# Optimization experiments

Measured on AMD Instinct MI355X. Metric: run time of the kernel, lower is better.

## Reference

```python
import jax, jax.numpy as jnp
import numpy as np

B, CIN, COUT, MODES, T = 64, 32, 32, 16, 1024
DT = 0.01  # uniform time-grid spacing (grid_x_train in the original repo)
SCALE = 1.0 / (CIN * COUT)


def setup_inputs() -> dict:
    key = jax.random.key(0)
    k = jax.random.split(key, 5)
    x = jax.random.normal(k[0], (B, CIN, T), dtype=jnp.float32)
    t = jnp.arange(T, dtype=jnp.float32) * np.float32(DT)
    # torch.rand with dtype=cfloat samples real and imag parts ~ U[0,1)
    pole_real = SCALE * jax.random.uniform(k[1], (CIN, COUT, MODES), dtype=jnp.float32)
    pole_imag = SCALE * jax.random.uniform(k[2], (CIN, COUT, MODES), dtype=jnp.float32)
    res_real = SCALE * jax.random.uniform(k[3], (CIN, COUT, MODES), dtype=jnp.float32)
    res_imag = SCALE * jax.random.uniform(k[4], (CIN, COUT, MODES), dtype=jnp.float32)
    return {"x": x, "t": t, "pole_real": pole_real, "pole_imag": pole_imag,
            "res_real": res_real, "res_imag": res_imag}


def reference(x, t, pole_real, pole_imag, res_real, res_imag):
    n = x.shape[-1]  # == T == t.shape[0]
    pole = (pole_real + 1j * pole_imag).astype(jnp.complex64)      # [i,o,m]
    residue = (res_real + 1j * res_imag).astype(jnp.complex64)     # [i,o,m]

    alpha = jnp.fft.fft(x)  # [b,i,T] complex64
    dt = t[1] - t[0]
    two_pi = np.float32(2.0 * np.pi)
    # lambda0 = fftfreq(T, dt) * 2*pi*1j  (fftfreq(T)/dt keeps dt traced-friendly)
    lam = ((jnp.fft.fftfreq(n).astype(jnp.float32) / dt) * two_pi * 1j).astype(jnp.complex64)  # [T]

    # Hw[x,i,o,k] = residue[i,o,k] / (lambda[x] - pole[i,o,k])
    Hw = residue[None, :, :, :] / (lam[:, None, None, None] - pole[None, :, :, :])  # [T,i,o,m]

    out1 = jnp.einsum('bix,xiok->box', alpha, Hw)    # [b,o,T]
    out2 = -jnp.einsum('bix,xiok->bok', alpha, Hw)   # [b,o,m]

    x1 = jnp.real(jnp.fft.ifft(out1, n=n))  # [b,o,T]

    # term2[i,o,m,z] = exp(pole[i,o,m] * t[z])
    term2 = jnp.exp(pole[:, :, :, None] * t.astype(jnp.complex64)[None, None, None, :])  # [i,o,m,T]
    # note: original einsum contracts out2's channel dim against term2's in-channel dim
    x2 = jnp.real(jnp.einsum('bix,ioxz->boz', out2, term2)) / n  # [b,o,T]

    return x1 + x2
```

## Files before the change

kernel.cpp:

```cpp
#include <hip/hip_runtime.h>

#define T_N   1024
#define B_N   64
#define CIN   32
#define COUT  32
#define MODES 16
#define DT    0.01f
#define PI_F  3.14159265358979323846f
#define W_SCALE 0.613592315154256f
#define W_NYQ  (-314.1592653589793f)

typedef short bf16x8 __attribute__((ext_vector_type(8)));
typedef float f32x4 __attribute__((ext_vector_type(4)));

__device__ __forceinline__ float fastrcp(float x) {
    float r;
    asm("v_rcp_f32 %0, %1" : "=v"(r) : "v"(x));
    return r;
}

__device__ __forceinline__ void bfsplit(float v, short* ph, short* pl) {
    unsigned int u = __float_as_uint(v);
    float lo = v - __uint_as_float(u & 0xFFFF0000u);
    *ph = (short)(u >> 16);
    *pl = (short)(__float_as_uint(lo) >> 16);
}

template <int SIGN>
__device__ __forceinline__ float2* fft1024_r4(float2* A, float2* B,
                                              const float2* TW, int tid) {
    float2* src = A;
    float2* dst = B;
    int m = 1;
#pragma unroll
    for (int s = 0; s < 5; ++s) {
        __syncthreads();
        int k  = tid & (m - 1);
        int jm = tid - k;
        float2 a = src[tid];
        float2 b = src[tid + 256];
        float2 c = src[tid + 512];
        float2 d = src[tid + 768];
        float2 t0 = make_float2(a.x + c.x, a.y + c.y);
        float2 t1 = make_float2(a.x - c.x, a.y - c.y);
        float2 t2 = make_float2(b.x + d.x, b.y + d.y);
        float2 t3 = make_float2(b.x - d.x, b.y - d.y);
        float2 it3 = (SIGN == 1) ? make_float2(-t3.y, t3.x)
                                 : make_float2(t3.y, -t3.x);
        float2 y0 = make_float2(t0.x + t2.x, t0.y + t2.y);
        float2 y2 = make_float2(t0.x - t2.x, t0.y - t2.y);
        float2 y1 = make_float2(t1.x + it3.x, t1.y + it3.y);
        float2 y3 = make_float2(t1.x - it3.x, t1.y - it3.y);
        float2 w1 = TW[jm];
        float2 w2 = TW[2 * jm];
        float2 w3 = TW[3 * jm];
        int ob = k + 4 * jm;
        dst[ob] = y0;
        dst[ob + m]     = make_float2(w1.x * y1.x - w1.y * y1.y,
                                      w1.x * y1.y + w1.y * y1.x);
        dst[ob + 2 * m] = make_float2(w2.x * y2.x - w2.y * y2.y,
                                      w2.x * y2.y + w2.y * y2.x);
        dst[ob + 3 * m] = make_float2(w3.x * y3.x - w3.y * y3.y,
                                      w3.x * y3.y + w3.y * y3.x);
        float2* t = src; src = dst; dst = t;
        m <<= 2;
    }
    __syncthreads();
    return src;
}

template <int SIGN>
__device__ __forceinline__ void build_tw4(float2* TW, int tid) {
#pragma unroll
    for (int r = 0; r < 4; ++r) {
        int a = tid + (r << 8);
        float sn, cs;
        __sincosf((float)SIGN * PI_F * (float)a * (1.0f / 512.0f), &sn, &cs);
        TW[a] = make_float2(cs, sn);
    }
}

__global__ __launch_bounds__(256) void k_fft_fwd(const float* __restrict__ x,
                                                 float2* __restrict__ alpha,
                                                 short* __restrict__ aHi,
                                                 short* __restrict__ aLo,
                                                 const float* __restrict__ pr,
                                                 const float* __restrict__ pim,
                                                 const float* __restrict__ rr,
                                                 const float* __restrict__ ri,
                                                 float4* __restrict__ pol4) {
    __shared__ float2 A[1024];
    __shared__ float2 Bb[1024];
    __shared__ float2 TW[1024];
    int row = blockIdx.x;
    int tid = threadIdx.x;
    build_tw4<-1>(TW, tid);
    const float* xr = x + (size_t)row * T_N;
#pragma unroll
    for (int r = 0; r < 4; ++r) {
        int j = tid + (r << 8);
        A[j] = make_float2(xr[j], 0.0f);
    }
    float2* R = fft1024_r4<-1>(A, Bb, TW, tid);
    float2* outp = alpha + (size_t)row * T_N;
#pragma unroll
    for (int r = 0; r < 4; ++r) {
        int j = tid + (r << 8);
        outp[j] = R[j];
    }
    size_t base = (size_t)row * 1024;
#pragma unroll
    for (int rr_ = 0; rr_ < 2; ++rr_) {
        int xj = tid + (rr_ << 8);
        float2 v = R[xj];
        float aR = v.x;
        float aI = (xj == 0) ? R[512].x : v.y;
        short h0, l0, h1, l1;
        bfsplit(aR, &h0, &l0);
        bfsplit(aI, &h1, &l1);
        aHi[base + xj * 2]     = h0;
        aHi[base + xj * 2 + 1] = h1;
        aLo[base + xj * 2]     = l0;
        aLo[base + xj * 2 + 1] = l1;
    }
    if (row < 64) {
        int idx = row * 256 + tid;
        pol4[idx] = make_float4(pr[idx], pim[idx], rr[idx], ri[idx]);
    }
}

__global__ __launch_bounds__(256) void k_transpose_hw(const float2* __restrict__ alpha,
                                                      unsigned int* __restrict__ aThU,
                                                      unsigned int* __restrict__ aTlU,
                                                      const float4* __restrict__ pol4,
                                                      float2* __restrict__ hw) {
    __shared__ float2 T[32 * 66];
    int bid = blockIdx.x;
    int tid = threadIdx.x;
    if (bid < 1024) {
        int i = bid >> 5, xt = bid & 31;
#pragma unroll
        for (int r = 0; r < 8; ++r) {
            int e = tid + (r << 8);
            int xx = e & 31, b = e >> 5;
            T[xx * 66 + b] = alpha[((size_t)(b * CIN + i)) * T_N + xt * 32 + xx];
        }
        __syncthreads();
#pragma unroll
        for (int r = 0; r < 8; ++r) {
            int e = tid + (r << 8);
            int b = e & 63, xx = e >> 6;
            float2 v = T[xx * 66 + b];
            short hR, lR, hI, lI;
            bfsplit(v.x, &hR, &lR);
            bfsplit(v.y, &hI, &lI);
            size_t idx = ((size_t)i * T_N + xt * 32 + xx) * B_N + b;
            aThU[idx] = (unsigned int)(unsigned short)hR |
                        ((unsigned int)(unsigned short)hI << 16);
            aTlU[idx] = (unsigned int)(unsigned short)lR |
                        ((unsigned int)(unsigned short)lI << 16);
        }
    } else {
        int xb = bid - 1024;
        int io0 = tid * 4;
        float wv[4];
#pragma unroll
        for (int xi = 0; xi < 4; ++xi) {
            int xg = xb * 4 + xi;
            int fx = xg - ((xg >= 512) ? 1024 : 0);
            wv[xi] = (float)fx * W_SCALE;
        }
        float accR[4][4], accI[4][4];
#pragma unroll
        for (int j = 0; j < 4; ++j) {
            const float4* pp = pol4 + (io0 + j) * 16;
            float4 p[16];
#pragma unroll
            for (int k = 0; k < 16; ++k) p[k] = pp[k];
#pragma unroll
            for (int xi = 0; xi < 4; ++xi) {
                float hr = 0.f, hi = 0.f;
#pragma unroll
                for (int k = 0; k < 16; ++k) {
                    float a = p[k].x, bI = p[k].y;
                    float d = wv[xi] - bI;
                    float inv = fastrcp(fmaf(d, d, a * a));
                    float vR = -a * inv, vI = -d * inv;
                    hr += p[k].z * vR - p[k].w * vI;
                    hi += p[k].z * vI + p[k].w * vR;
                }
                accR[xi][j] = hr;
                accI[xi][j] = hi;
            }
        }
#pragma unroll
        for (int xi = 0; xi < 4; ++xi) {
            float4* dst = (float4*)(hw + (size_t)(xb * 4 + xi) * 1024 + io0);
            dst[0] = make_float4(accR[xi][0], accI[xi][0], accR[xi][1], accI[xi][1]);
            dst[1] = make_float4(accR[xi][2], accI[xi][2], accR[xi][3], accI[xi][3]);
        }
    }
}

__global__ __launch_bounds__(256) void k_out1(const unsigned int* __restrict__ aThU,
                                              const unsigned int* __restrict__ aTlU,
                                              const float2* __restrict__ hw,
                                              float2* __restrict__ out1tmp) {
    __shared__ float sARe[32 * 64];
    __shared__ float sAIm[32 * 64];
    int x = blockIdx.x;
    int tid = threadIdx.x;

#pragma unroll
    for (int r = 0; r < 4; ++r) {
        int e = tid + (r << 8);
        int i = e >> 5, bp = e & 31;
        size_t base = ((size_t)i * T_N + x) * B_N + bp * 2;
        uint2 uh = *(const uint2*)&aThU[base];
        uint2 ul = *(const uint2*)&aTlU[base];
        float r0 = __uint_as_float(uh.x << 16) + __uint_as_float(ul.x << 16);
        float i0 = __uint_as_float(uh.x & 0xFFFF0000u) + __uint_as_float(ul.x & 0xFFFF0000u);
        float r1 = __uint_as_float(uh.y << 16) + __uint_as_float(ul.y << 16);
        float i1 = __uint_as_float(uh.y & 0xFFFF0000u) + __uint_as_float(ul.y & 0xFFFF0000u);
        *(float2*)&sARe[i * 64 + bp * 2] = make_float2(r0, r1);
        *(float2*)&sAIm[i * 64 + bp * 2] = make_float2(i0, i1);
    }
    __syncthreads();

    int o = tid & 31, bg = tid >> 5;
    const float2* hrow = hw + (size_t)x * 1024 + o;
    float accR[8] = {}, accI[8] = {};
#pragma unroll 4
    for (int i = 0; i < CIN; ++i) {
        float2 h = hrow[i * 32];
        float4 ar0 = *(const float4*)&sARe[i * 64 + bg * 8];
        float4 ar1 = *(const float4*)&sARe[i * 64 + bg * 8 + 4];
        float4 ai0 = *(const float4*)&sAIm[i * 64 + bg * 8];
        float4 ai1 = *(const float4*)&sAIm[i * 64 + bg * 8 + 4];
        float aR[8] = {ar0.x, ar0.y, ar0.z, ar0.w, ar1.x, ar1.y, ar1.z, ar1.w};
        float aI[8] = {ai0.x, ai0.y, ai0.z, ai0.w, ai1.x, ai1.y, ai1.z, ai1.w};
#pragma unroll
        for (int bb = 0; bb < 8; ++bb) {
            accR[bb] += aR[bb] * h.x - aI[bb] * h.y;
            accI[bb] += aR[bb] * h.y + aI[bb] * h.x;
        }
    }
#pragma unroll
    for (int bb = 0; bb < 8; ++bb) {
        out1tmp[(size_t)x * 2048 + (bg * 8 + bb) * 32 + o] =
            make_float2(accR[bb], accI[bb]);
    }
}

#define ABROW 40
__global__ __launch_bounds__(256) void k_out2m(const short* __restrict__ aHi,
                                               const short* __restrict__ aLo,
                                               const float* __restrict__ pr,
                                               const float* __restrict__ pim,
                                               const float* __restrict__ rr,
                                               const float* __restrict__ ri,
                                               float* __restrict__ partial) {
    __shared__ short sAh[64 * ABROW], sAl[64 * ABROW];
    __shared__ short sBh[64 * ABROW], sBl[64 * ABROW];
    __shared__ float sPol[4][32];

    const int nb = blockIdx.x, xh = blockIdx.y, i = blockIdx.z;
    const int tid = threadIdx.x;
    const int w = tid >> 6, l = tid & 63;
    const int r = l & 15, hg = l >> 4;

    if (tid < 32) {
        int o = nb * 2 + (tid >> 4), k = tid & 15;
        int pidx = (i * COUT + o) * MODES + k;
        sPol[0][tid] = pr[pidx]; sPol[1][tid] = pim[pidx];
        sPol[2][tid] = rr[pidx]; sPol[3][tid] = ri[pidx];
    }
    __syncthreads();

    f32x4 acc0 = {0.f, 0.f, 0.f, 0.f};
    f32x4 acc1 = {0.f, 0.f, 0.f, 0.f};
    f32x4 acc2 = {0.f, 0.f, 0.f, 0.f};
    f32x4 acc3 = {0.f, 0.f, 0.f, 0.f};

    const int sb = tid >> 2;
    const int sc = (tid & 3) * 8;
    const size_t abase = ((size_t)sb * CIN + i) * 1024 + (size_t)xh * 512;

    const int bn = tid & 63, bh = tid >> 6;
    const int bok = bn >> 1, bcomp = bn & 1;
    const float pa = sPol[0][bok], pb = sPol[1][bok];
    const float prr_ = sPol[2][bok], pri_ = sPol[3][bok];
    const float K_d  = pa * pa - pb * pb;
    const float mKe  = -2.0f * pa * pb;
    const float K_e2 = (2.0f * pa * pb) * (2.0f * pa * pb);
    const float prx2 = 2.0f * (pa * prr_ - pb * pri_);
    const float piy2 = 2.0f * (pa * pri_ + pb * prr_);
    const float A1 = bcomp ? piy2 : prx2;
    const float B1 = bcomp ? prx2 : -piy2;
    const float A2 = bcomp ? pri_ : prr_;
    const float B2 = bcomp ? prr_ : -pri_;

    for (int ks = 0; ks < 16; ++ks) {
        __syncthreads();
        *(float4*)&sAh[sb * ABROW + sc] = *(const float4*)&aHi[abase + ks * 32 + sc];
        *(float4*)&sAl[sb * ABROW + sc] = *(const float4*)&aLo[abase + ks * 32 + sc];
        {
            bf16x8 vh, vl;
#pragma unroll
            for (int j4 = 0; j4 < 4; ++j4) {
                int xl = bh * 4 + j4;
                int xg = xh * 256 + ks * 16 + xl;
                float v1, v2;
                if (xg == 0) {
                    float s1 = pa * pa + pb * pb;
                    float q1r = pa / s1, q1i = -pb / s1;
                    float c1r = prr_ * q1r - pri_ * q1i;
                    float c1i = prr_ * q1i + pri_ * q1r;
                    float dr = -pa, di = W_NYQ - pb;
                    float s2 = dr * dr + di * di;
                    float q2r = dr / s2, q2i = -di / s2;
                    float c2r = -(prr_ * q2r - pri_ * q2i);
                    float c2i = -(prr_ * q2i + pri_ * q2r);
                    v1 = bcomp ? c1i : c1r;
                    v2 = bcomp ? c2i : c2r;
                } else {
                    float wv = (float)xg * W_SCALE;
                    float denr = fmaf(wv, wv, K_d);
                    float s = fmaf(denr, denr, K_e2);
                    float inv = fastrcp(s);
                    float qr = denr * inv, qi = mKe * inv;
                    v1 = A1 * qr + B1 * qi;
                    float rq = A2 * qr + B2 * qi;
                    v2 = -2.0f * wv * rq;
                }
                short h1, l1, h2, l2;
                bfsplit(v1, &h1, &l1);
                bfsplit(v2, &h2, &l2);
                vh[j4 * 2] = h1; vh[j4 * 2 + 1] = h2;
                vl[j4 * 2] = l1; vl[j4 * 2 + 1] = l2;
            }
            *(bf16x8*)&sBh[bn * ABROW + bh * 8] = vh;
            *(bf16x8*)&sBl[bn * ABROW + bh * 8] = vl;
        }
        __syncthreads();

        bf16x8 bhf = *(bf16x8*)&sBh[(w * 16 + r) * ABROW + hg * 8];
        bf16x8 blf = *(bf16x8*)&sBl[(w * 16 + r) * ABROW + hg * 8];
        {
            bf16x8 ah = *(bf16x8*)&sAh[(0 * 16 + r) * ABROW + hg * 8];
            bf16x8 al = *(bf16x8*)&sAl[(0 * 16 + r) * ABROW + hg * 8];
            acc0 = __builtin_amdgcn_mfma_f32_16x16x32_bf16(ah, bhf, acc0, 0, 0, 0);
            acc0 = __builtin_amdgcn_mfma_f32_16x16x32_bf16(al, bhf, acc0, 0, 0, 0);
            acc0 = __builtin_amdgcn_mfma_f32_16x16x32_bf16(ah, blf, acc0, 0, 0, 0);
        }
        {
            bf16x8 ah = *(bf16x8*)&sAh[(1 * 16 + r) * ABROW + hg * 8];
            bf16x8 al = *(bf16x8*)&sAl[(1 * 16 + r) * ABROW + hg * 8];
            acc1 = __builtin_amdgcn_mfma_f32_16x16x32_bf16(ah, bhf, acc1, 0, 0, 0);
            acc1 = __builtin_amdgcn_mfma_f32_16x16x32_bf16(al, bhf, acc1, 0, 0, 0);
            acc1 = __builtin_amdgcn_mfma_f32_16x16x32_bf16(ah, blf, acc1, 0, 0, 0);
        }
        {
            bf16x8 ah = *(bf16x8*)&sAh[(2 * 16 + r) * ABROW + hg * 8];
            bf16x8 al = *(bf16x8*)&sAl[(2 * 16 + r) * ABROW + hg * 8];
            acc2 = __builtin_amdgcn_mfma_f32_16x16x32_bf16(ah, bhf, acc2, 0, 0, 0);
            acc2 = __builtin_amdgcn_mfma_f32_16x16x32_bf16(al, bhf, acc2, 0, 0, 0);
            acc2 = __builtin_amdgcn_mfma_f32_16x16x32_bf16(ah, blf, acc2, 0, 0, 0);
        }
        {
            bf16x8 ah = *(bf16x8*)&sAh[(3 * 16 + r) * ABROW + hg * 8];
            bf16x8 al = *(bf16x8*)&sAl[(3 * 16 + r) * ABROW + hg * 8];
            acc3 = __builtin_amdgcn_mfma_f32_16x16x32_bf16(ah, bhf, acc3, 0, 0, 0);
            acc3 = __builtin_amdgcn_mfma_f32_16x16x32_bf16(al, bhf, acc3, 0, 0, 0);
            acc3 = __builtin_amdgcn_mfma_f32_16x16x32_bf16(ah, blf, acc3, 0, 0, 0);
        }
    }

    int chunk = i * 2 + xh;
    int n = nb * 64 + w * 16 + r;
    float* dst = partial + (size_t)chunk * (B_N * 1024) + n;
#pragma unroll
    for (int reg = 0; reg < 4; ++reg) {
        dst[(0 * 16 + hg * 4 + reg) * 1024] = acc0[reg];
        dst[(1 * 16 + hg * 4 + reg) * 1024] = acc1[reg];
        dst[(2 * 16 + hg * 4 + reg) * 1024] = acc2[reg];
        dst[(3 * 16 + hg * 4 + reg) * 1024] = acc3[reg];
    }
}

__global__ __launch_bounds__(256) void k_reduce(const float4* __restrict__ p,
                                                short4* __restrict__ aXh,
                                                short4* __restrict__ aXl,
                                                int nchunk) {
    int f = blockIdx.x * 256 + threadIdx.x;
    float4 s = make_float4(0.f, 0.f, 0.f, 0.f);
    for (int c = 0; c < nchunk; ++c) {
        float4 v = p[(size_t)c * 16384 + f];
        s.x += v.x; s.y += v.y; s.z += v.z; s.w += v.w;
    }
    short4 h, l;
    bfsplit(s.x, &h.x, &l.x);
    bfsplit(s.y, &h.y, &l.y);
    bfsplit(s.z, &h.z, &l.z);
    bfsplit(s.w, &h.w, &l.w);
    aXh[f] = h;
    aXl[f] = l;
}

__global__ __launch_bounds__(256) void k_transpose_o1(const float2* __restrict__ out1tmp,
                                                      float2* __restrict__ out1T) {
    __shared__ float2 T[64 * 33];
    int blk = blockIdx.x;
    int bot = blk >> 5, xt = blk & 31;
    int tid = threadIdx.x;
#pragma unroll
    for (int r = 0; r < 8; ++r) {
        int e = tid + (r << 8);
        int j = e & 63, xr = e >> 6;
        T[j * 33 + xr] = out1tmp[((size_t)(xt * 32 + xr)) * 2048 + bot * 64 + j];
    }
    __syncthreads();
#pragma unroll
    for (int r = 0; r < 8; ++r) {
        int e = tid + (r << 8);
        int xx = e & 31, j = e >> 5;
        out1T[((size_t)(bot * 64 + j)) * T_N + xt * 32 + xx] = T[j * 33 + xx];
    }
}

__global__ __launch_bounds__(256) void k_ifft(const float2* __restrict__ out1T,
                                              float* __restrict__ outp) {
    __shared__ float2 A[1024];
    __shared__ float2 Bb[1024];
    __shared__ float2 TW[1024];
    int row = blockIdx.x;
    int tid = threadIdx.x;
    build_tw4<1>(TW, tid);
    const float2* src = out1T + (size_t)row * T_N;
#pragma unroll
    for (int r = 0; r < 4; ++r) {
        int j = tid + (r << 8);
        A[j] = src[j];
    }
    float2* R = fft1024_r4<1>(A, Bb, TW, tid);
    float* dst = outp + (size_t)row * T_N;
    const float inv_n = 1.0f / (float)T_N;
#pragma unroll
    for (int r = 0; r < 4; ++r) {
        int j = tid + (r << 8);
        dst[j] = R[j].x * inv_n;
    }
}

__global__ __launch_bounds__(256) void k_x2m(const short* __restrict__ aXh,
                                             const short* __restrict__ aXl,
                                             const float* __restrict__ pr,
                                             const float* __restrict__ pim,
                                             float* __restrict__ outp) {
    __shared__ short sAh[64 * ABROW], sAl[64 * ABROW];
    __shared__ short sBh[64 * ABROW], sBl[64 * ABROW];
    __shared__ float s_pr[512], s_pim[512];

    const int zb = blockIdx.x, o = blockIdx.y;
    const int tid = threadIdx.x;
    const int w = tid >> 6, l = tid & 63;
    const int r = l & 15, hg = l >> 4;

#pragma unroll
    for (int rr_ = 0; rr_ < 2; ++rr_) {
        int cm = tid + (rr_ << 8);
        int c = cm >> 4, m = cm & 15;
        int pidx = (c * COUT + o) * MODES + m;
        s_pr[cm] = pr[pidx];
        s_pim[cm] = pim[pidx];
    }
    __syncthreads();

    f32x4 acc0 = {0.f, 0.f, 0.f, 0.f};
    f32x4 acc1 = {0.f, 0.f, 0.f, 0.f};
    f32x4 acc2 = {0.f, 0.f, 0.f, 0.f};
    f32x4 acc3 = {0.f, 0.f, 0.f, 0.f};

    const int sb = tid >> 2;
    const int sc = (tid & 3) * 8;
    const float z0f = (float)(zb * 64);

    const int bz = tid & 63, bh = tid >> 6;
    const float tz = (z0f + (float)bz) * DT;

    for (int ks = 0; ks < 32; ++ks) {
        __syncthreads();
        *(float4*)&sAh[sb * ABROW + sc] = *(const float4*)&aXh[sb * 1024 + ks * 32 + sc];
        *(float4*)&sAl[sb * ABROW + sc] = *(const float4*)&aXl[sb * 1024 + ks * 32 + sc];
        {
            bf16x8 vh, vl;
#pragma unroll
            for (int j4 = 0; j4 < 4; ++j4) {
                int cml = bh * 4 + j4;
                int cm = ks * 16 + cml;
                float gr = s_pr[cm], gi = s_pim[cm];
                float er = __expf(gr * tz);
                float sn, cn;
                __sincosf(gi * tz, &sn, &cn);
                short h1, l1, h2, l2;
                bfsplit(er * cn,  &h1, &l1);
                bfsplit(-er * sn, &h2, &l2);
                vh[j4 * 2] = h1; vh[j4 * 2 + 1] = h2;
                vl[j4 * 2] = l1; vl[j4 * 2 + 1] = l2;
            }
            *(bf16x8*)&sBh[bz * ABROW + bh * 8] = vh;
            *(bf16x8*)&sBl[bz * ABROW + bh * 8] = vl;
        }
        __syncthreads();

        bf16x8 bhf = *(bf16x8*)&sBh[(w * 16 + r) * ABROW + hg * 8];
        bf16x8 blf = *(bf16x8*)&sBl[(w * 16 + r) * ABROW + hg * 8];
        {
            bf16x8 ah = *(bf16x8*)&sAh[(0 * 16 + r) * ABROW + hg * 8];
            bf16x8 al = *(bf16x8*)&sAl[(0 * 16 + r) * ABROW + hg * 8];
            acc0 = __builtin_amdgcn_mfma_f32_16x16x32_bf16(ah, bhf, acc0, 0, 0, 0);
            acc0 = __builtin_amdgcn_mfma_f32_16x16x32_bf16(al, bhf, acc0, 0, 0, 0);
            acc0 = __builtin_amdgcn_mfma_f32_16x16x32_bf16(ah, blf, acc0, 0, 0, 0);
        }
        {
            bf16x8 ah = *(bf16x8*)&sAh[(1 * 16 + r) * ABROW + hg * 8];
            bf16x8 al = *(bf16x8*)&sAl[(1 * 16 + r) * ABROW + hg * 8];
            acc1 = __builtin_amdgcn_mfma_f32_16x16x32_bf16(ah, bhf, acc1, 0, 0, 0);
            acc1 = __builtin_amdgcn_mfma_f32_16x16x32_bf16(al, bhf, acc1, 0, 0, 0);
            acc1 = __builtin_amdgcn_mfma_f32_16x16x32_bf16(ah, blf, acc1, 0, 0, 0);
        }
        {
            bf16x8 ah = *(bf16x8*)&sAh[(2 * 16 + r) * ABROW + hg * 8];
            bf16x8 al = *(bf16x8*)&sAl[(2 * 16 + r) * ABROW + hg * 8];
            acc2 = __builtin_amdgcn_mfma_f32_16x16x32_bf16(ah, bhf, acc2, 0, 0, 0);
            acc2 = __builtin_amdgcn_mfma_f32_16x16x32_bf16(al, bhf, acc2, 0, 0, 0);
            acc2 = __builtin_amdgcn_mfma_f32_16x16x32_bf16(ah, blf, acc2, 0, 0, 0);
        }
        {
            bf16x8 ah = *(bf16x8*)&sAh[(3 * 16 + r) * ABROW + hg * 8];
            bf16x8 al = *(bf16x8*)&sAl[(3 * 16 + r) * ABROW + hg * 8];
            acc3 = __builtin_amdgcn_mfma_f32_16x16x32_bf16(ah, bhf, acc3, 0, 0, 0);
            acc3 = __builtin_amdgcn_mfma_f32_16x16x32_bf16(al, bhf, acc3, 0, 0, 0);
            acc3 = __builtin_amdgcn_mfma_f32_16x16x32_bf16(ah, blf, acc3, 0, 0, 0);
        }
    }

    const float inv_n = 1.0f / (float)T_N;
    size_t base = (size_t)o * T_N + zb * 64 + w * 16 + r;
#pragma unroll
    for (int reg = 0; reg < 4; ++reg) {
        size_t i0 = base + (size_t)(0 * 16 + hg * 4 + reg) * (COUT * T_N);
        size_t i1 = base + (size_t)(1 * 16 + hg * 4 + reg) * (COUT * T_N);
        size_t i2 = base + (size_t)(2 * 16 + hg * 4 + reg) * (COUT * T_N);
        size_t i3 = base + (size_t)(3 * 16 + hg * 4 + reg) * (COUT * T_N);
        outp[i0] += acc0[reg] * inv_n;
        outp[i1] += acc1[reg] * inv_n;
        outp[i2] += acc2[reg] * inv_n;
        outp[i3] += acc3[reg] * inv_n;
    }
}

extern "C" void kernel_launch(void* const* d_in, const int* in_sizes, int n_in,
                              void* d_out, int out_size, void* d_ws, size_t ws_size,
                              hipStream_t stream) {
    const float* x   = (const float*)d_in[0];
    const float* pr  = (const float*)d_in[2];
    const float* pim = (const float*)d_in[3];
    const float* rr  = (const float*)d_in[4];
    const float* ri  = (const float*)d_in[5];
    float* outp = (float*)d_out;

    char* ws = (char*)d_ws;
    const size_t MB = 1024 * 1024;
    const size_t KB = 1024;
    float2*       alpha  = (float2*)ws;
    unsigned int* aThU   = (unsigned int*)(ws + 16 * MB);
    unsigned int* aTlU   = (unsigned int*)(ws + 24 * MB);
    short*        aXh    = (short*)(ws + 32 * MB);
    short*        aXl    = (short*)(ws + 32 * MB + 128 * KB);
    float4*       pol4   = (float4*)(ws + 32 * MB + 512 * KB);
    short*        aHi    = (short*)(ws + 33 * MB);
    short*        aLo    = (short*)(ws + 37 * MB);
    float2*       hw     = (float2*)(ws + 41 * MB);
    float*        o2part  = (float*)ws;
    float2*       out1tmp = (float2*)ws;
    float2*       out1T   = (float2*)(ws + 16 * MB);

    k_fft_fwd     <<<B_N * CIN, 256, 0, stream>>>(x, alpha, aHi, aLo,
                                                  pr, pim, rr, ri, pol4);
    k_transpose_hw<<<1280, 256, 0, stream>>>(alpha, aThU, aTlU, pol4, hw);
    k_out2m       <<<dim3(16, 2, 32), 256, 0, stream>>>(aHi, aLo,
                                                        pr, pim, rr, ri, o2part);
    k_reduce      <<<64, 256, 0, stream>>>((const float4*)o2part,
                                           (short4*)aXh, (short4*)aXl, 64);
    k_out1        <<<T_N, 256, 0, stream>>>(aThU, aTlU, hw, out1tmp);
    k_transpose_o1<<<32 * 32, 256, 0, stream>>>(out1tmp, out1T);
    k_ifft        <<<B_N * COUT, 256, 0, stream>>>(out1T, outp);
    k_x2m         <<<dim3(16, 32), 256, 0, stream>>>(aXh, aXl, pr, pim, outp);
}
```

Before: 136.5 us.

## Merge independent stages into shared launches to cut kernel count

Result: faster. 118.9 us (-12.9%).

```diff
diff --git a/kernel.cpp b/kernel.cpp
--- a/kernel.cpp
+++ b/kernel.cpp
@@ -199,56 +199,6 @@
             dst[0] = make_float4(accR[xi][0], accI[xi][0], accR[xi][1], accI[xi][1]);
             dst[1] = make_float4(accR[xi][2], accI[xi][2], accR[xi][3], accI[xi][3]);
         }
-    }
-}
-
-__global__ __launch_bounds__(256) void k_out1(const unsigned int* __restrict__ aThU,
-                                              const unsigned int* __restrict__ aTlU,
-                                              const float2* __restrict__ hw,
-                                              float2* __restrict__ out1tmp) {
-    __shared__ float sARe[32 * 64];
-    __shared__ float sAIm[32 * 64];
-    int x = blockIdx.x;
-    int tid = threadIdx.x;
-
-#pragma unroll
-    for (int r = 0; r < 4; ++r) {
-        int e = tid + (r << 8);
-        int i = e >> 5, bp = e & 31;
-        size_t base = ((size_t)i * T_N + x) * B_N + bp * 2;
-        uint2 uh = *(const uint2*)&aThU[base];
-        uint2 ul = *(const uint2*)&aTlU[base];
-        float r0 = __uint_as_float(uh.x << 16) + __uint_as_float(ul.x << 16);
-        float i0 = __uint_as_float(uh.x & 0xFFFF0000u) + __uint_as_float(ul.x & 0xFFFF0000u);
-        float r1 = __uint_as_float(uh.y << 16) + __uint_as_float(ul.y << 16);
-        float i1 = __uint_as_float(uh.y & 0xFFFF0000u) + __uint_as_float(ul.y & 0xFFFF0000u);
-        *(float2*)&sARe[i * 64 + bp * 2] = make_float2(r0, r1);
-        *(float2*)&sAIm[i * 64 + bp * 2] = make_float2(i0, i1);
-    }
-    __syncthreads();
-
-    int o = tid & 31, bg = tid >> 5;
-    const float2* hrow = hw + (size_t)x * 1024 + o;
-    float accR[8] = {}, accI[8] = {};
-#pragma unroll 4
-    for (int i = 0; i < CIN; ++i) {
-        float2 h = hrow[i * 32];
-        float4 ar0 = *(const float4*)&sARe[i * 64 + bg * 8];
-        float4 ar1 = *(const float4*)&sARe[i * 64 + bg * 8 + 4];
-        float4 ai0 = *(const float4*)&sAIm[i * 64 + bg * 8];
-        float4 ai1 = *(const float4*)&sAIm[i * 64 + bg * 8 + 4];
-        float aR[8] = {ar0.x, ar0.y, ar0.z, ar0.w, ar1.x, ar1.y, ar1.z, ar1.w};
-        float aI[8] = {ai0.x, ai0.y, ai0.z, ai0.w, ai1.x, ai1.y, ai1.z, ai1.w};
-#pragma unroll
-        for (int bb = 0; bb < 8; ++bb) {
-            accR[bb] += aR[bb] * h.x - aI[bb] * h.y;
-            accI[bb] += aR[bb] * h.y + aI[bb] * h.x;
-        }
-    }
-#pragma unroll
-    for (int bb = 0; bb < 8; ++bb) {
-        out1tmp[(size_t)x * 2048 + (bg * 8 + bb) * 32 + o] =
-            make_float2(accR[bb], accI[bb]);
     }
 }
 
@@ -388,81 +338,114 @@
     }
 }
 
-__global__ __launch_bounds__(256) void k_reduce(const float4* __restrict__ p,
-                                                short4* __restrict__ aXh,
-                                                short4* __restrict__ aXl,
-                                                int nchunk) {
-    int f = blockIdx.x * 256 + threadIdx.x;
-    float4 s = make_float4(0.f, 0.f, 0.f, 0.f);
-    for (int c = 0; c < nchunk; ++c) {
-        float4 v = p[(size_t)c * 16384 + f];
-        s.x += v.x; s.y += v.y; s.z += v.z; s.w += v.w;
-    }
-    short4 h, l;
-    bfsplit(s.x, &h.x, &l.x);
-    bfsplit(s.y, &h.y, &l.y);
-    bfsplit(s.z, &h.z, &l.z);
-    bfsplit(s.w, &h.w, &l.w);
-    aXh[f] = h;
-    aXl[f] = l;
-}
-
-__global__ __launch_bounds__(256) void k_transpose_o1(const float2* __restrict__ out1tmp,
-                                                      float2* __restrict__ out1T) {
-    __shared__ float2 T[64 * 33];
-    int blk = blockIdx.x;
-    int bot = blk >> 5, xt = blk & 31;
+__global__ __launch_bounds__(256) void k_out1_reduce(const unsigned int* __restrict__ aThU,
+                                                     const unsigned int* __restrict__ aTlU,
+                                                     const float2* __restrict__ hw,
+                                                     float2* __restrict__ out1tmp,
+                                                     const float4* __restrict__ p,
+                                                     short4* __restrict__ aXh,
+                                                     short4* __restrict__ aXl) {
+    __shared__ float sARe[32 * 64];
+    __shared__ float sAIm[32 * 64];
+    int bid = blockIdx.x;
     int tid = threadIdx.x;
-#pragma unroll
-    for (int r = 0; r < 8; ++r) {
+    if (bid >= 1024) {
+        int f = (bid - 1024) * 256 + tid;
+        float4 s = make_float4(0.f, 0.f, 0.f, 0.f);
+        for (int c = 0; c < 64; ++c) {
+            float4 v = p[(size_t)c * 16384 + f];
+            s.x += v.x; s.y += v.y; s.z += v.z; s.w += v.w;
+        }
+        short4 h, l;
+        bfsplit(s.x, &h.x, &l.x);
+        bfsplit(s.y, &h.y, &l.y);
+        bfsplit(s.z, &h.z, &l.z);
+        bfsplit(s.w, &h.w, &l.w);
+        aXh[f] = h;
+        aXl[f] = l;
+        return;
+    }
+    int x = bid;
+#pragma unroll
+    for (int r = 0; r < 4; ++r) {
         int e = tid + (r << 8);
-        int j = e & 63, xr = e >> 6;
-        T[j * 33 + xr] = out1tmp[((size_t)(xt * 32 + xr)) * 2048 + bot * 64 + j];
+        int i = e >> 5, bp = e & 31;
+        size_t base = ((size_t)i * T_N + x) * B_N + bp * 2;
+        uint2 uh = *(const uint2*)&aThU[base];
+        uint2 ul = *(const uint2*)&aTlU[base];
+        float r0 = __uint_as_float(uh.x << 16) + __uint_as_float(ul.x << 16);
+        float i0 = __uint_as_float(uh.x & 0xFFFF0000u) + __uint_as_float(ul.x & 0xFFFF0000u);
+        float r1 = __uint_as_float(uh.y << 16) + __uint_as_float(ul.y << 16);
+        float i1 = __uint_as_float(uh.y & 0xFFFF0000u) + __uint_as_float(ul.y & 0xFFFF0000u);
+        *(float2*)&sARe[i * 64 + bp * 2] = make_float2(r0, r1);
+        *(float2*)&sAIm[i * 64 + bp * 2] = make_float2(i0, i1);
     }
     __syncthreads();
-#pragma unroll
-    for (int r = 0; r < 8; ++r) {
-        int e = tid + (r << 8);
-        int xx = e & 31, j = e >> 5;
-        out1T[((size_t)(bot * 64 + j)) * T_N + xt * 32 + xx] = T[j * 33 + xx];
-    }
-}
-
-__global__ __launch_bounds__(256) void k_ifft(const float2* __restrict__ out1T,
-                                              float* __restrict__ outp) {
-    __shared__ float2 A[1024];
-    __shared__ float2 Bb[1024];
-    __shared__ float2 TW[1024];
-    int row = blockIdx.x;
+
+    int o = tid & 31, bg = tid >> 5;
+    const float2* hrow = hw + (size_t)x * 1024 + o;
+    float accR[8] = {}, accI[8] = {};
+#pragma unroll 4
+    for (int i = 0; i < CIN; ++i) {
+        float2 h = hrow[i * 32];
+        float4 ar0 = *(const float4*)&sARe[i * 64 + bg * 8];
+        float4 ar1 = *(const float4*)&sARe[i * 64 + bg * 8 + 4];
+        float4 ai0 = *(const float4*)&sAIm[i * 64 + bg * 8];
+        float4 ai1 = *(const float4*)&sAIm[i * 64 + bg * 8 + 4];
+        float aR[8] = {ar0.x, ar0.y, ar0.z, ar0.w, ar1.x, ar1.y, ar1.z, ar1.w};
+        float aI[8] = {ai0.x, ai0.y, ai0.z, ai0.w, ai1.x, ai1.y, ai1.z, ai1.w};
+#pragma unroll
+        for (int bb = 0; bb < 8; ++bb) {
+            accR[bb] += aR[bb] * h.x - aI[bb] * h.y;
+            accI[bb] += aR[bb] * h.y + aI[bb] * h.x;
+        }
+    }
+#pragma unroll
+    for (int bb = 0; bb < 8; ++bb) {
+        out1tmp[(size_t)x * 2048 + (bg * 8 + bb) * 32 + o] =
+            make_float2(accR[bb], accI[bb]);
+    }
+}
+
+__global__ __launch_bounds__(256) void k_to1_x2m(const float2* __restrict__ out1tmp,
+                                                 float2* __restrict__ out1T,
+                                                 const short* __restrict__ aXhS,
+                                                 const short* __restrict__ aXlS,
+                                                 const float* __restrict__ pr,
+                                                 const float* __restrict__ pim,
+                                                 float* __restrict__ outp) {
+    __shared__ __align__(16) char SMEM[24576];
+    int bid = blockIdx.x;
     int tid = threadIdx.x;
-    build_tw4<1>(TW, tid);
-    const float2* src = out1T + (size_t)row * T_N;
-#pragma unroll
-    for (int r = 0; r < 4; ++r) {
-        int j = tid + (r << 8);
-        A[j] = src[j];
-    }
-    float2* R = fft1024_r4<1>(A, Bb, TW, tid);
-    float* dst = outp + (size_t)row * T_N;
-    const float inv_n = 1.0f / (float)T_N;
-#pragma unroll
-    for (int r = 0; r < 4; ++r) {
-        int j = tid + (r << 8);
-        dst[j] = R[j].x * inv_n;
-    }
-}
-
-__global__ __launch_bounds__(256) void k_x2m(const short* __restrict__ aXh,
-                                             const short* __restrict__ aXl,
-                                             const float* __restrict__ pr,
-                                             const float* __restrict__ pim,
-                                             float* __restrict__ outp) {
-    __shared__ short sAh[64 * ABROW], sAl[64 * ABROW];
-    __shared__ short sBh[64 * ABROW], sBl[64 * ABROW];
-    __shared__ float s_pr[512], s_pim[512];
-
-    const int zb = blockIdx.x, o = blockIdx.y;
-    const int tid = threadIdx.x;
+
+    if (bid < 1024) {
+        float2* T = (float2*)SMEM;
+        int bot = bid >> 5, xt = bid & 31;
+#pragma unroll
+        for (int r = 0; r < 8; ++r) {
+            int e = tid + (r << 8);
+            int j = e & 63, xr = e >> 6;
+            T[j * 33 + xr] = out1tmp[((size_t)(xt * 32 + xr)) * 2048 + bot * 64 + j];
+        }
+        __syncthreads();
+#pragma unroll
+        for (int r = 0; r < 8; ++r) {
+            int e = tid + (r << 8);
+            int xx = e & 31, j = e >> 5;
+            out1T[((size_t)(bot * 64 + j)) * T_N + xt * 32 + xx] = T[j * 33 + xx];
+        }
+        return;
+    }
+
+    short* sAh = (short*)SMEM;
+    short* sAl = sAh + 64 * ABROW;
+    short* sBh = sAl + 64 * ABROW;
+    short* sBl = sBh + 64 * ABROW;
+    float* s_pr = (float*)(SMEM + 20480);
+    float* s_pim = s_pr + 512;
+
+    int zz = bid - 1024;
+    const int zb = zz & 15, o = zz >> 4;
     const int w = tid >> 6, l = tid & 63;
     const int r = l & 15, hg = l >> 4;
 
@@ -490,8 +473,8 @@
 
     for (int ks = 0; ks < 32; ++ks) {
         __syncthreads();
-        *(float4*)&sAh[sb * ABROW + sc] = *(const float4*)&aXh[sb * 1024 + ks * 32 + sc];
-        *(float4*)&sAl[sb * ABROW + sc] = *(const float4*)&aXl[sb * 1024 + ks * 32 + sc];
+        *(float4*)&sAh[sb * ABROW + sc] = *(const float4*)&aXhS[sb * 1024 + ks * 32 + sc];
+        *(float4*)&sAl[sb * ABROW + sc] = *(const float4*)&aXlS[sb * 1024 + ks * 32 + sc];
         {
             bf16x8 vh, vl;
 #pragma unroll
@@ -553,10 +536,34 @@
         size_t i1 = base + (size_t)(1 * 16 + hg * 4 + reg) * (COUT * T_N);
         size_t i2 = base + (size_t)(2 * 16 + hg * 4 + reg) * (COUT * T_N);
         size_t i3 = base + (size_t)(3 * 16 + hg * 4 + reg) * (COUT * T_N);
-        outp[i0] += acc0[reg] * inv_n;
-        outp[i1] += acc1[reg] * inv_n;
-        outp[i2] += acc2[reg] * inv_n;
-        outp[i3] += acc3[reg] * inv_n;
+        outp[i0] = acc0[reg] * inv_n;
+        outp[i1] = acc1[reg] * inv_n;
+        outp[i2] = acc2[reg] * inv_n;
+        outp[i3] = acc3[reg] * inv_n;
+    }
+}
+
+__global__ __launch_bounds__(256) void k_ifft(const float2* __restrict__ out1T,
+                                              float* __restrict__ outp) {
+    __shared__ float2 A[1024];
+    __shared__ float2 Bb[1024];
+    __shared__ float2 TW[1024];
+    int row = blockIdx.x;
+    int tid = threadIdx.x;
+    build_tw4<1>(TW, tid);
+    const float2* src = out1T + (size_t)row * T_N;
+#pragma unroll
+    for (int r = 0; r < 4; ++r) {
+        int j = tid + (r << 8);
+        A[j] = src[j];
+    }
+    float2* R = fft1024_r4<1>(A, Bb, TW, tid);
+    float* dst = outp + (size_t)row * T_N;
+    const float inv_n = 1.0f / (float)T_N;
+#pragma unroll
+    for (int r = 0; r < 4; ++r) {
+        int j = tid + (r << 8);
+        dst[j] += R[j].x * inv_n;
     }
 }
 
@@ -582,8 +589,8 @@
     short*        aHi    = (short*)(ws + 33 * MB);
     short*        aLo    = (short*)(ws + 37 * MB);
     float2*       hw     = (float2*)(ws + 41 * MB);
+    float2*       out1tmp = (float2*)(ws + 49 * MB);
     float*        o2part  = (float*)ws;
-    float2*       out1tmp = (float2*)ws;
     float2*       out1T   = (float2*)(ws + 16 * MB);
 
     k_fft_fwd     <<<B_N * CIN, 256, 0, stream>>>(x, alpha, aHi, aLo,
@@ -591,10 +598,10 @@
     k_transpose_hw<<<1280, 256, 0, stream>>>(alpha, aThU, aTlU, pol4, hw);
     k_out2m       <<<dim3(16, 2, 32), 256, 0, stream>>>(aHi, aLo,
                                                         pr, pim, rr, ri, o2part);
-    k_reduce      <<<64, 256, 0, stream>>>((const float4*)o2part,
-                                           (short4*)aXh, (short4*)aXl, 64);
-    k_out1        <<<T_N, 256, 0, stream>>>(aThU, aTlU, hw, out1tmp);
-    k_transpose_o1<<<32 * 32, 256, 0, stream>>>(out1tmp, out1T);
+    k_out1_reduce <<<1088, 256, 0, stream>>>(aThU, aTlU, hw, out1tmp,
+                                             (const float4*)o2part,
+                                             (short4*)aXh, (short4*)aXl);
+    k_to1_x2m     <<<1536, 256, 0, stream>>>(out1tmp, out1T, aXh, aXl,
+                                             pr, pim, outp);
     k_ifft        <<<B_N * COUT, 256, 0, stream>>>(out1T, outp);
-    k_x2m         <<<dim3(16, 32), 256, 0, stream>>>(aXh, aXl, pr, pim, outp);
-}
+}
```
